# Kernel tuning notes

Measured on AMD Instinct MI355X. Metric: run time of the kernel, lower is better.

The kernel has to match this reference:

```python
import jax, jax.numpy as jnp
import numpy as np

N = 16384
D_IN = 1024
HID = [512, 512, 256]
N_PAIRS = 100000
N_CLS = 3


def setup_inputs() -> dict:
    key = jax.random.key(0)
    ks = jax.random.split(key, 16)
    x = jax.random.normal(ks[0], (N, D_IN), dtype=jnp.float32)
    adj = jax.random.uniform(ks[1], (N, N), dtype=jnp.float32) / N  # dense normalized adjacency
    tf_idx = jax.random.randint(ks[2], (N_PAIRS,), 0, N)
    gene_idx = jax.random.randint(ks[3], (N_PAIRS,), 0, N)
    # GCN layer weights
    W0 = jax.random.normal(ks[4], (D_IN, HID[0]), dtype=jnp.float32) / np.sqrt(D_IN)
    b0 = jnp.zeros((HID[0],), dtype=jnp.float32)
    W1 = jax.random.normal(ks[5], (HID[0], HID[1]), dtype=jnp.float32) / np.sqrt(HID[0])
    b1 = jnp.zeros((HID[1],), dtype=jnp.float32)
    W2 = jax.random.normal(ks[6], (HID[1], HID[2]), dtype=jnp.float32) / np.sqrt(HID[1])
    b2 = jnp.zeros((HID[2],), dtype=jnp.float32)
    # MLP head: Linear(2*256 -> 256), GELU, Linear(256 -> 3)
    Wh1 = jax.random.normal(ks[7], (2 * HID[2], HID[2]), dtype=jnp.float32) / np.sqrt(2 * HID[2])
    bh1 = jnp.zeros((HID[2],), dtype=jnp.float32)
    Wh2 = jax.random.normal(ks[8], (HID[2], N_CLS), dtype=jnp.float32) / np.sqrt(HID[2])
    bh2 = jnp.zeros((N_CLS,), dtype=jnp.float32)
    return {"x": x, "adj": adj, "tf_idx": tf_idx, "gene_idx": gene_idx,
            "W0": W0, "b0": b0, "W1": W1, "b1": b1, "W2": W2, "b2": b2,
            "Wh1": Wh1, "bh1": bh1, "Wh2": Wh2, "bh2": bh2}


def reference(x, adj, tf_idx, gene_idx, W0, b0, W1, b1, W2, b2, Wh1, bh1, Wh2, bh2):
    # GCNConv: out = adj @ (x @ W) + b; ReLU between layers (dropout off in eval)
    h = jax.nn.relu(adj @ (x @ W0) + b0)          # [N, 512]
    h = jax.nn.relu(adj @ (h @ W1) + b1)          # [N, 512]
    emb = adj @ (h @ W2) + b2                      # [N, 256]
    pair = jnp.concatenate([emb[tf_idx], emb[gene_idx]], axis=-1)  # [P, 512]
    hdn = jax.nn.gelu(pair @ Wh1 + bh1, approximate=False)          # [P, 256]
    logits = hdn @ Wh2 + bh2                                        # [P, 3]
    return logits
```

## Files before the change

### kernel.cpp

```cpp
#include <hip/hip_runtime.h>
#include <hip/hip_bf16.h>
#include <stdint.h>


using f32x4  = __attribute__((ext_vector_type(4))) float;
using bf16x8 = __attribute__((ext_vector_type(8))) __bf16;
using u16x8  = __attribute__((ext_vector_type(8))) unsigned short;
using u16x4  = __attribute__((ext_vector_type(4))) unsigned short;

static __device__ __forceinline__ unsigned short f2bf(float f) {
  unsigned u = __builtin_bit_cast(unsigned, f);
  u += 0x7FFFu + ((u >> 16) & 1u);
  return (unsigned short)(u >> 16);
}
static __device__ __forceinline__ float bf2f(unsigned short h) {
  unsigned u = ((unsigned)h) << 16;
  return __builtin_bit_cast(float, u);
}
static __device__ __forceinline__ void gload_lds16(const void* g, void* l) {
  __builtin_amdgcn_global_load_lds((__attribute__((address_space(1))) void*)(void*)g,
                                   (__attribute__((address_space(3))) void*)l,
                                   16, 0, 0);
}


__global__ void tcvt_kernel(const float* __restrict__ in,
                            unsigned short* __restrict__ outp, int K, int Nf) {
  int id = blockIdx.x * 256 + threadIdx.x;
  if (id >= K * Nf) return;
  int k = id % K, nf = id / K;
  outp[id] = f2bf(in[(size_t)k * Nf + nf]);
}

__global__ void cvt_bf16_kernel(const float* __restrict__ in,
                                unsigned short* __restrict__ outp, size_t n) {
  size_t i = ((size_t)blockIdx.x * blockDim.x + threadIdx.x) * 8;
  size_t stride = (size_t)gridDim.x * blockDim.x * 8;
  for (; i + 8 <= n; i += stride) {
    const float4* p = (const float4*)(in + i);
    float4 a = p[0], b = p[1];
    u16x8 v;
    v[0] = f2bf(a.x); v[1] = f2bf(a.y); v[2] = f2bf(a.z); v[3] = f2bf(a.w);
    v[4] = f2bf(b.x); v[5] = f2bf(b.y); v[6] = f2bf(b.z); v[7] = f2bf(b.w);
    *(u16x8*)(outp + i) = v;
  }
}

template <int NPART, bool RELU>
__global__ void reduceK_kernel(const float* __restrict__ Pp, const float* __restrict__ bias,
                               unsigned short* __restrict__ outp, int MN, int Nmask) {
  int i = (blockIdx.x * 256 + threadIdx.x) * 4;
  if (i >= MN) return;
  float4 s = *(const float4*)(Pp + i);
#pragma unroll
  for (int p = 1; p < NPART; ++p) {
    float4 v = *(const float4*)(Pp + (size_t)p * MN + i);
    s.x += v.x; s.y += v.y; s.z += v.z; s.w += v.w;
  }
  int col = i & Nmask;
  float r0 = s.x + bias[col + 0];
  float r1 = s.y + bias[col + 1];
  float r2 = s.z + bias[col + 2];
  float r3 = s.w + bias[col + 3];
  if (RELU) {
    r0 = fmaxf(r0, 0.0f); r1 = fmaxf(r1, 0.0f);
    r2 = fmaxf(r2, 0.0f); r3 = fmaxf(r3, 0.0f);
  }
  u16x4 o;
  o[0] = f2bf(r0); o[1] = f2bf(r1); o[2] = f2bf(r2); o[3] = f2bf(r3);
  *(u16x4*)(outp + i) = o;
}

__global__ __launch_bounds__(512, 1)
void gemm256(const unsigned short* __restrict__ A, const unsigned short* __restrict__ Bt,
             float* __restrict__ Pp, int M, int N, int K, int nbx, int Klen) {
  __shared__ __align__(16) unsigned short As[4 * 256 * 32];
  __shared__ __align__(16) unsigned short Bs[4 * 256 * 32];
  const int t = threadIdx.x, l = t & 63, w = t >> 6;

  int wg = blockIdx.x;
  const int cpx = gridDim.x >> 3;
  wg = (wg & 7) * cpx + (wg >> 3);
  const int mb = wg / nbx, nb = wg % nbx;
  const int kc = blockIdx.y;
  const int koff = kc * Klen;
  const int wr = w >> 2, wc = w & 3;
  const int fr = l & 15, fq = l >> 4;

  const int srow = t >> 2;
  const int sk0  = (t & 3) * 8;
  const unsigned short* AgR = A  + (size_t)(mb * 256 + srow) * K + koff + sk0;
  const unsigned short* BgR = Bt + (size_t)(nb * 256 + srow) * K + koff + sk0;
  unsigned short* AsL = As + t * 8;
  unsigned short* BsL = Bs + t * 8;

  const int NT = Klen >> 5;

#pragma unroll
  for (int s = 0; s < 3; ++s) {
    gload_lds16(AgR + s * 32, AsL + s * 8192);
    gload_lds16(AgR + (size_t)128 * K + s * 32, AsL + s * 8192 + 4096);
    gload_lds16(BgR + s * 32, BsL + s * 8192);
    gload_lds16(BgR + (size_t)128 * K + s * 32, BsL + s * 8192 + 4096);
  }
  asm volatile("s_waitcnt vmcnt(8)" ::: "memory");
  __builtin_amdgcn_sched_barrier(0);
  __builtin_amdgcn_s_barrier();

  f32x4 acc[8][4] = {};
  for (int tt = 0; tt < NT; ++tt) {
    const int buf = tt & 3;
    const int sb  = (tt + 3) & 3;
    const unsigned short* Ab = As + buf * 8192;
    const unsigned short* Bb = Bs + buf * 8192;
    const bool stg = (tt + 3) < NT;
    const unsigned short* AgS = AgR + (size_t)(tt + 3) * 32;
    const unsigned short* BgS = BgR + (size_t)(tt + 3) * 32;

    bf16x8 bfr[4], af[4];
#pragma unroll
    for (int ni = 0; ni < 4; ++ni)
      bfr[ni] = *(const bf16x8*)&Bb[(wc * 64 + ni * 16 + fr) * 32 + fq * 8];
#pragma unroll
    for (int mi = 0; mi < 4; ++mi)
      af[mi] = *(const bf16x8*)&Ab[(wr * 128 + mi * 16 + fr) * 32 + fq * 8];
    if (stg) {
      gload_lds16(AgS, AsL + sb * 8192);
      gload_lds16(AgS + (size_t)128 * K, AsL + sb * 8192 + 4096);
    }
    __builtin_amdgcn_sched_barrier(0);
    __builtin_amdgcn_s_barrier();
    asm volatile("s_waitcnt lgkmcnt(0)" ::: "memory");
    __builtin_amdgcn_sched_barrier(0);
    __builtin_amdgcn_s_setprio(1);
#pragma unroll
    for (int mi = 0; mi < 4; ++mi)
#pragma unroll
      for (int ni = 0; ni < 4; ++ni)
        acc[mi][ni] = __builtin_amdgcn_mfma_f32_16x16x32_bf16(af[mi], bfr[ni],
                                                              acc[mi][ni], 0, 0, 0);
    __builtin_amdgcn_s_setprio(0);
    __builtin_amdgcn_sched_barrier(0);
    __builtin_amdgcn_s_barrier();

    bf16x8 ag[4];
#pragma unroll
    for (int mi = 0; mi < 4; ++mi)
      ag[mi] = *(const bf16x8*)&Ab[(wr * 128 + (mi + 4) * 16 + fr) * 32 + fq * 8];
    if (stg) {
      gload_lds16(BgS, BsL + sb * 8192);
      gload_lds16(BgS + (size_t)128 * K, BsL + sb * 8192 + 4096);
    }
    __builtin_amdgcn_sched_barrier(0);
    __builtin_amdgcn_s_barrier();
    asm volatile("s_waitcnt lgkmcnt(0)" ::: "memory");
    __builtin_amdgcn_sched_barrier(0);
    __builtin_amdgcn_s_setprio(1);
#pragma unroll
    for (int mi = 0; mi < 4; ++mi)
#pragma unroll
      for (int ni = 0; ni < 4; ++ni)
        acc[mi + 4][ni] = __builtin_amdgcn_mfma_f32_16x16x32_bf16(ag[mi], bfr[ni],
                                                                  acc[mi + 4][ni], 0, 0, 0);
    __builtin_amdgcn_s_setprio(0);
    __builtin_amdgcn_sched_barrier(0);

    if (tt + 4 <= NT) {
      asm volatile("s_waitcnt vmcnt(8)" ::: "memory");
    } else if (tt + 3 == NT) {
      asm volatile("s_waitcnt vmcnt(4)" ::: "memory");
    } else {
      asm volatile("s_waitcnt vmcnt(0)" ::: "memory");
    }
    __builtin_amdgcn_sched_barrier(0);
    __builtin_amdgcn_s_barrier();
  }

  float* C = Pp + (size_t)kc * M * N;
  const int growb = mb * 256 + wr * 128 + fq * 4;
  const int gcolb = nb * 256 + wc * 64 + fr;
#pragma unroll
  for (int mi = 0; mi < 8; ++mi) {
    int row = growb + mi * 16;
#pragma unroll
    for (int ni = 0; ni < 4; ++ni) {
      int col = gcolb + ni * 16;
      f32x4 v = acc[mi][ni];
#pragma unroll
      for (int r = 0; r < 4; ++r)
        C[(size_t)(row + r) * N + col] = v[r];
    }
  }
}

template <int EP, bool ABF16>
__global__ __launch_bounds__(256, 2)
void gemm_bt(const void* __restrict__ Av, const unsigned short* __restrict__ Bt,
             void* __restrict__ Cout, const float* __restrict__ bias,
             int M, int N, int K, int nbx, int Klen) {
  __shared__ __align__(16) unsigned short As[128 * 64];
  __shared__ __align__(16) unsigned short Bs[128 * 64];
  const int t = threadIdx.x;
  const int l = t & 63;
  const int w = t >> 6;

  int wg = blockIdx.x;
  const int cpx = gridDim.x >> 3;
  wg = (wg & 7) * cpx + (wg >> 3);
  const int mb = wg / nbx, nb = wg % nbx;
  const int kc = blockIdx.y;
  const int koff = kc * Klen;

  const int wr = w >> 1, wc = w & 1;
  f32x4 acc[4][4] = {};

  const int srow = w * 8 + (l >> 3);
  const int sk0  = 8 * ((l & 7) ^ (l >> 3));
  const unsigned short* Bg = Bt + (size_t)(nb * 128 + srow) * K + koff + sk0;
  unsigned short* BsL = Bs + w * 512 + l * 8;
  unsigned short* AsL = As + w * 512 + l * 8;

  const unsigned short* Ag16 = nullptr;
  const float* Ag32 = nullptr;
  unsigned short* AsWr = nullptr;
  int ak = 0, axm = 0;
  if constexpr (ABF16) {
    Ag16 = (const unsigned short*)Av + (size_t)(mb * 128 + srow) * K + koff + sk0;
  } else {
    const int ar = t >> 1;
    ak = (t & 1) * 32;
    axm = (ar & 7) << 3;
    Ag32 = (const float*)Av + (size_t)(mb * 128 + ar) * K + koff + ak;
    AsWr = As + ar * 64;
  }

  const int fr = l & 15, fq = l >> 4;
  const int rxor = (fr & 7) << 3;

  const int steps = Klen >> 6;
  for (int kb = 0; kb < steps; ++kb) {
#pragma unroll
    for (int i = 0; i < 4; ++i)
      gload_lds16(Bg + (size_t)i * 32 * K, BsL + i * 2048);
    Bg += 64;
    if constexpr (ABF16) {
#pragma unroll
      for (int i = 0; i < 4; ++i)
        gload_lds16(Ag16 + (size_t)i * 32 * K, AsL + i * 2048);
      Ag16 += 64;
    } else {
#pragma unroll
      for (int q = 0; q < 4; ++q) {
        float4 c0 = ((const float4*)Ag32)[q * 2];
        float4 c1 = ((const float4*)Ag32)[q * 2 + 1];
        u16x8 v;
        v[0] = f2bf(c0.x); v[1] = f2bf(c0.y); v[2] = f2bf(c0.z); v[3] = f2bf(c0.w);
        v[4] = f2bf(c1.x); v[5] = f2bf(c1.y); v[6] = f2bf(c1.z); v[7] = f2bf(c1.w);
        *(u16x8*)&AsWr[(ak + q * 8) ^ axm] = v;
      }
      Ag32 += 64;
    }
    __syncthreads();

    bf16x8 af[2][4], bfr[2][4];
#pragma unroll
    for (int kk = 0; kk < 2; ++kk) {
#pragma unroll
      for (int mi = 0; mi < 4; ++mi) {
        int arow = wr * 64 + mi * 16 + fr;
        af[kk][mi] = *(const bf16x8*)&As[arow * 64 + ((kk * 32 + fq * 8) ^ rxor)];
      }
#pragma unroll
      for (int ni = 0; ni < 4; ++ni) {
        int brow = wc * 64 + ni * 16 + fr;
        bfr[kk][ni] = *(const bf16x8*)&Bs[brow * 64 + ((kk * 32 + fq * 8) ^ rxor)];
      }
    }
#pragma unroll
    for (int kk = 0; kk < 2; ++kk)
#pragma unroll
      for (int mi = 0; mi < 4; ++mi)
#pragma unroll
        for (int ni = 0; ni < 4; ++ni)
          acc[mi][ni] = __builtin_amdgcn_mfma_f32_16x16x32_bf16(af[kk][mi], bfr[kk][ni],
                                                                acc[mi][ni], 0, 0, 0);
    __syncthreads();
  }

  const int r0 = fq * 4;
  const int c0 = fr;
  const int growb = mb * 128 + wr * 64 + r0;
  const int gcolb = nb * 128 + wc * 64 + c0;
  if constexpr (EP == 0) {
    unsigned short* Ct = (unsigned short*)Cout;
#pragma unroll
    for (int ni = 0; ni < 4; ++ni) {
      int col = gcolb + ni * 16;
#pragma unroll
      for (int mi = 0; mi < 4; ++mi) {
        int row = growb + mi * 16;
        f32x4 v = acc[mi][ni];
        u16x4 o;
        o[0] = f2bf(v[0]); o[1] = f2bf(v[1]); o[2] = f2bf(v[2]); o[3] = f2bf(v[3]);
        *(u16x4*)&Ct[(size_t)col * M + row] = o;
      }
    }
  } else if constexpr (EP == 1) {
    unsigned short* C = (unsigned short*)Cout;
#pragma unroll
    for (int ni = 0; ni < 4; ++ni) {
      int col = gcolb + ni * 16;
      float b = bias[col];
#pragma unroll
      for (int mi = 0; mi < 4; ++mi) {
        int row = growb + mi * 16;
        f32x4 v = acc[mi][ni];
#pragma unroll
        for (int r = 0; r < 4; ++r)
          C[(size_t)(row + r) * N + col] = f2bf(fmaxf(v[r] + b, 0.0f));
      }
    }
  } else {
    float* C = (float*)Cout + (size_t)kc * M * N;
#pragma unroll
    for (int ni = 0; ni < 4; ++ni) {
      int col = gcolb + ni * 16;
#pragma unroll
      for (int mi = 0; mi < 4; ++mi) {
        int row = growb + mi * 16;
        f32x4 v = acc[mi][ni];
#pragma unroll
        for (int r = 0; r < 4; ++r)
          C[(size_t)(row + r) * N + col] = v[r];
      }
    }
  }
}

__global__ __launch_bounds__(256, 2)
void head_kernel(const unsigned short* __restrict__ EMB, const int* __restrict__ tf,
                 const int* __restrict__ gi, const unsigned short* __restrict__ Wh1t,
                 const float* __restrict__ bh1, const float* __restrict__ Wh2,
                 const float* __restrict__ bh2, float* __restrict__ out, int P) {
  __shared__ __align__(16) union SU {
    struct { unsigned short As[64 * 64]; unsigned short Bs[256 * 64]; } s;
    unsigned short hdn[64 * 264];
  } u;
  __shared__ float wh2s[256 * 3];
  const int t = threadIdx.x, l = t & 63, w = t >> 6;
  const int pb = blockIdx.x;

  wh2s[t]       = Wh2[t];
  wh2s[t + 256] = Wh2[t + 256];
  wh2s[t + 512] = Wh2[t + 512];

  const int srow = w * 8 + (l >> 3);
  const int sk0  = 8 * ((l & 7) ^ (l >> 3));
  size_t tfo[2], gio[2];
#pragma unroll
  for (int i = 0; i < 2; ++i) {
    int p = pb * 64 + i * 32 + srow;
    if (p >= P) p = P - 1;
    tfo[i] = (size_t)tf[p] * 256;
    gio[i] = (size_t)gi[p] * 256;
  }
  const unsigned short* BgB = Wh1t + (size_t)srow * 512 + sk0;
  unsigned short* AsL = u.s.As + w * 512 + l * 8;
  unsigned short* BsL = u.s.Bs + w * 512 + l * 8;

  const int fr = l & 15, fq = l >> 4;
  const int rxor = (fr & 7) << 3;

  f32x4 acc[4][4] = {};
  for (int kb = 0; kb < 8; ++kb) {
    const int klo = (kb & 3) * 64 + sk0;
#pragma unroll
    for (int i = 0; i < 2; ++i)
      gload_lds16(EMB + ((kb < 4) ? tfo[i] : gio[i]) + klo, AsL + i * 2048);
#pragma unroll
    for (int i = 0; i < 8; ++i)
      gload_lds16(BgB + (size_t)i * 32 * 512 + kb * 64, BsL + i * 2048);
    __syncthreads();

    bf16x8 af[2][4], bfr[2][4];
#pragma unroll
    for (int kk = 0; kk < 2; ++kk) {
#pragma unroll
      for (int mi = 0; mi < 4; ++mi) {
        int arow = mi * 16 + fr;
        af[kk][mi] = *(const bf16x8*)&u.s.As[arow * 64 + ((kk * 32 + fq * 8) ^ rxor)];
      }
#pragma unroll
      for (int ni = 0; ni < 4; ++ni) {
        int brow = w * 64 + ni * 16 + fr;
        bfr[kk][ni] = *(const bf16x8*)&u.s.Bs[brow * 64 + ((kk * 32 + fq * 8) ^ rxor)];
      }
    }
#pragma unroll
    for (int kk = 0; kk < 2; ++kk)
#pragma unroll
      for (int mi = 0; mi < 4; ++mi)
#pragma unroll
        for (int ni = 0; ni < 4; ++ni)
          acc[mi][ni] = __builtin_amdgcn_mfma_f32_16x16x32_bf16(af[kk][mi], bfr[kk][ni],
                                                                acc[mi][ni], 0, 0, 0);
    __syncthreads();
  }

  const int r0 = fq * 4, c0 = fr;
#pragma unroll
  for (int ni = 0; ni < 4; ++ni) {
    int col = w * 64 + ni * 16 + c0;
    float b = bh1[col];
#pragma unroll
    for (int mi = 0; mi < 4; ++mi) {
      int row = mi * 16 + r0;
      f32x4 v = acc[mi][ni];
#pragma unroll
      for (int r = 0; r < 4; ++r) {
        float xv = v[r] + b;
        float g = 0.5f * xv * (1.0f + erff(xv * 0.70710678118f));
        u.hdn[(row + r) * 264 + col] = f2bf(g);
      }
    }
  }
  __syncthreads();

  const int pl = w * 16 + (l >> 2);
  const int pg = pb * 64 + pl;
  const int ks = (l & 3) * 64;
  float a0 = 0.f, a1 = 0.f, a2 = 0.f;
  const unsigned short* hr = u.hdn + pl * 264 + ks;
#pragma unroll
  for (int kq = 0; kq < 8; ++kq) {
    u16x8 hv = *(const u16x8*)(hr + kq * 8);
#pragma unroll
    for (int j = 0; j < 8; ++j) {
      float h = bf2f(hv[j]);
      int k = ks + kq * 8 + j;
      a0 = fmaf(h, wh2s[k * 3 + 0], a0);
      a1 = fmaf(h, wh2s[k * 3 + 1], a1);
      a2 = fmaf(h, wh2s[k * 3 + 2], a2);
    }
  }
  a0 += __shfl_xor(a0, 1); a0 += __shfl_xor(a0, 2);
  a1 += __shfl_xor(a1, 1); a1 += __shfl_xor(a1, 2);
  a2 += __shfl_xor(a2, 1); a2 += __shfl_xor(a2, 2);
  if ((l & 3) == 0 && pg < P) {
    out[(size_t)pg * 3 + 0] = a0 + bh2[0];
    out[(size_t)pg * 3 + 1] = a1 + bh2[1];
    out[(size_t)pg * 3 + 2] = a2 + bh2[2];
  }
}


extern "C" void kernel_launch(void* const* d_in, const int* in_sizes, int n_in,
                              void* d_out, int out_size, void* d_ws, size_t ws_size,
                              hipStream_t stream) {
  const float* x   = (const float*)d_in[0];
  const float* adj = (const float*)d_in[1];
  const int*   tf  = (const int*)d_in[2];
  const int*   gi  = (const int*)d_in[3];
  const float* W0  = (const float*)d_in[4];
  const float* b0  = (const float*)d_in[5];
  const float* W1  = (const float*)d_in[6];
  const float* b1  = (const float*)d_in[7];
  const float* W2  = (const float*)d_in[8];
  const float* b2  = (const float*)d_in[9];
  const float* Wh1 = (const float*)d_in[10];
  const float* bh1 = (const float*)d_in[11];
  const float* Wh2 = (const float*)d_in[12];
  const float* bh2 = (const float*)d_in[13];
  float* out = (float*)d_out;

  const int NN = 16384;
  const int P = in_sizes[2];

  char* ws = (char*)d_ws;
  size_t off = 0;
  auto alloc = [&](size_t bytes) -> char* {
    char* p = ws + off;
    off += (bytes + 255) & ~(size_t)255;
    return p;
  };
  unsigned short* W0t  = (unsigned short*)alloc((size_t)512 * 1024 * 2);
  unsigned short* W1t  = (unsigned short*)alloc((size_t)512 * 512 * 2);
  unsigned short* W2t  = (unsigned short*)alloc((size_t)256 * 512 * 2);
  unsigned short* Wh1t = (unsigned short*)alloc((size_t)256 * 512 * 2);
  unsigned short* Tt   = (unsigned short*)alloc((size_t)512 * NN * 2);
  unsigned short* H    = (unsigned short*)alloc((size_t)NN * 512 * 2);
  unsigned short* EMB  = (unsigned short*)alloc((size_t)NN * 256 * 2);
  float*          Pp   = (float*)alloc((size_t)2 * NN * 512 * 4);
  size_t base_end = off;

  bool useAdjB = false;
  unsigned short* adjb = nullptr;
  if (ws_size >= base_end + (size_t)NN * NN * 2) {
    adjb = (unsigned short*)alloc((size_t)NN * NN * 2);
    useAdjB = true;
  }

  tcvt_kernel<<<dim3((1024 * 512 + 255) / 256), 256, 0, stream>>>(W0, W0t, 1024, 512);
  tcvt_kernel<<<dim3((512 * 512 + 255) / 256), 256, 0, stream>>>(W1, W1t, 512, 512);
  tcvt_kernel<<<dim3((512 * 256 + 255) / 256), 256, 0, stream>>>(W2, W2t, 512, 256);
  tcvt_kernel<<<dim3((512 * 256 + 255) / 256), 256, 0, stream>>>(Wh1, Wh1t, 512, 256);
  if (useAdjB)
    cvt_bf16_kernel<<<4096, 256, 0, stream>>>(adj, adjb, (size_t)NN * NN);

  gemm_bt<0, false><<<dim3(512), 256, 0, stream>>>(x, W0t, Tt, nullptr,
                                                   NN, 512, 1024, 4, 1024);
  if (useAdjB) {
    gemm256<<<dim3(128, 2), 512, 0, stream>>>(adjb, Tt, Pp, NN, 512, NN, 2, NN / 2);
    reduceK_kernel<2, true><<<dim3(8192), 256, 0, stream>>>(Pp, b0, H, NN * 512, 511);
  } else {
    gemm_bt<1, false><<<dim3(512), 256, 0, stream>>>(adj, Tt, H, b0,
                                                     NN, 512, NN, 4, NN);
  }
  gemm_bt<0, true><<<dim3(512), 256, 0, stream>>>(H, W1t, Tt, nullptr,
                                                  NN, 512, 512, 4, 512);
  if (useAdjB) {
    gemm256<<<dim3(128, 2), 512, 0, stream>>>(adjb, Tt, Pp, NN, 512, NN, 2, NN / 2);
    reduceK_kernel<2, true><<<dim3(8192), 256, 0, stream>>>(Pp, b1, H, NN * 512, 511);
  } else {
    gemm_bt<1, false><<<dim3(512), 256, 0, stream>>>(adj, Tt, H, b1,
                                                     NN, 512, NN, 4, NN);
  }
  gemm_bt<0, true><<<dim3(256), 256, 0, stream>>>(H, W2t, Tt, nullptr,
                                                  NN, 256, 512, 2, 512);
  if (useAdjB) {
    gemm256<<<dim3(64, 4), 512, 0, stream>>>(adjb, Tt, Pp, NN, 256, NN, 1, NN / 4);
    reduceK_kernel<4, false><<<dim3(4096), 256, 0, stream>>>(Pp, b2, EMB, NN * 256, 255);
  } else {
    gemm_bt<3, false><<<dim3(256, 2), 256, 0, stream>>>(adj, Tt, Pp, nullptr,
                                                        NN, 256, NN, 2, NN / 2);
    reduceK_kernel<2, false><<<dim3(4096), 256, 0, stream>>>(Pp, b2, EMB, NN * 256, 255);
  }
  head_kernel<<<dim3((P + 63) / 64), 256, 0, stream>>>(EMB, tf, gi, Wh1t, bh1,
                                                       Wh2, bh2, out, P);
}
```

Measured before the change: 1.289 ms.

## Software-pipeline LDS fragment reads and cut GEMM loop to one barrier per K-step

New measurement: 1.311 ms. About the same (+1.7%).

```diff
diff --git a/kernel.cpp b/kernel.cpp
--- a/kernel.cpp
+++ b/kernel.cpp
@@ -96,85 +96,87 @@
 
   const int NT = Klen >> 5;
 
-#pragma unroll
-  for (int s = 0; s < 3; ++s) {
-    gload_lds16(AgR + s * 32, AsL + s * 8192);
-    gload_lds16(AgR + (size_t)128 * K + s * 32, AsL + s * 8192 + 4096);
-    gload_lds16(BgR + s * 32, BsL + s * 8192);
-    gload_lds16(BgR + (size_t)128 * K + s * 32, BsL + s * 8192 + 4096);
-  }
-  asm volatile("s_waitcnt vmcnt(8)" ::: "memory");
+  const int aoff = (wr * 128 + fr) * 32 + fq * 8;
+  const int boff = (wc * 64 + fr) * 32 + fq * 8;
+
+#define STAGE_A(s)                                                            \
+  { gload_lds16(AgR + (size_t)(s) * 32, AsL + ((s) & 3) * 8192);              \
+    gload_lds16(AgR + (size_t)128 * K + (size_t)(s) * 32,                     \
+                AsL + ((s) & 3) * 8192 + 4096); }
+#define STAGE_B(s)                                                            \
+  { gload_lds16(BgR + (size_t)(s) * 32, BsL + ((s) & 3) * 8192);              \
+    gload_lds16(BgR + (size_t)128 * K + (size_t)(s) * 32,                     \
+                BsL + ((s) & 3) * 8192 + 4096); }
+#define READ_B(dst, u)                                                        \
+  _Pragma("unroll")                                                           \
+  for (int ni = 0; ni < 4; ++ni)                                              \
+    dst[ni] = *(const bf16x8*)&Bs[((u) & 3) * 8192 + boff + ni * 512];
+#define READ_A03(dst, u)                                                      \
+  _Pragma("unroll")                                                           \
+  for (int mi = 0; mi < 4; ++mi)                                              \
+    dst[mi] = *(const bf16x8*)&As[((u) & 3) * 8192 + aoff + mi * 512];
+#define READ_A47(dst, u)                                                      \
+  _Pragma("unroll")                                                           \
+  for (int mi = 0; mi < 4; ++mi)                                              \
+    dst[mi] = *(const bf16x8*)&As[((u) & 3) * 8192 + aoff + 2048 + mi * 512];
+
+#pragma unroll
+  for (int s = 0; s < 3; ++s) { STAGE_A(s); STAGE_B(s); }
+  asm volatile("s_waitcnt vmcnt(4)" ::: "memory");
   __builtin_amdgcn_sched_barrier(0);
   __builtin_amdgcn_s_barrier();
 
+  bf16x8 bA[4], aA[4], bB[4], aB[4], a47[4];
+  READ_B(bA, 0);
+  READ_A03(aA, 0);
+
   f32x4 acc[8][4] = {};
-  for (int tt = 0; tt < NT; ++tt) {
-    const int buf = tt & 3;
-    const int sb  = (tt + 3) & 3;
-    const unsigned short* Ab = As + buf * 8192;
-    const unsigned short* Bb = Bs + buf * 8192;
-    const bool stg = (tt + 3) < NT;
-    const unsigned short* AgS = AgR + (size_t)(tt + 3) * 32;
-    const unsigned short* BgS = BgR + (size_t)(tt + 3) * 32;
-
-    bf16x8 bfr[4], af[4];
-#pragma unroll
-    for (int ni = 0; ni < 4; ++ni)
-      bfr[ni] = *(const bf16x8*)&Bb[(wc * 64 + ni * 16 + fr) * 32 + fq * 8];
-#pragma unroll
-    for (int mi = 0; mi < 4; ++mi)
-      af[mi] = *(const bf16x8*)&Ab[(wr * 128 + mi * 16 + fr) * 32 + fq * 8];
-    if (stg) {
-      gload_lds16(AgS, AsL + sb * 8192);
-      gload_lds16(AgS + (size_t)128 * K, AsL + sb * 8192 + 4096);
-    }
-    __builtin_amdgcn_sched_barrier(0);
-    __builtin_amdgcn_s_barrier();
-    asm volatile("s_waitcnt lgkmcnt(0)" ::: "memory");
-    __builtin_amdgcn_sched_barrier(0);
-    __builtin_amdgcn_s_setprio(1);
-#pragma unroll
-    for (int mi = 0; mi < 4; ++mi)
-#pragma unroll
-      for (int ni = 0; ni < 4; ++ni)
-        acc[mi][ni] = __builtin_amdgcn_mfma_f32_16x16x32_bf16(af[mi], bfr[ni],
-                                                              acc[mi][ni], 0, 0, 0);
-    __builtin_amdgcn_s_setprio(0);
-    __builtin_amdgcn_sched_barrier(0);
-    __builtin_amdgcn_s_barrier();
-
-    bf16x8 ag[4];
-#pragma unroll
-    for (int mi = 0; mi < 4; ++mi)
-      ag[mi] = *(const bf16x8*)&Ab[(wr * 128 + (mi + 4) * 16 + fr) * 32 + fq * 8];
-    if (stg) {
-      gload_lds16(BgS, BsL + sb * 8192);
-      gload_lds16(BgS + (size_t)128 * K, BsL + sb * 8192 + 4096);
-    }
-    __builtin_amdgcn_sched_barrier(0);
-    __builtin_amdgcn_s_barrier();
-    asm volatile("s_waitcnt lgkmcnt(0)" ::: "memory");
-    __builtin_amdgcn_sched_barrier(0);
-    __builtin_amdgcn_s_setprio(1);
-#pragma unroll
-    for (int mi = 0; mi < 4; ++mi)
-#pragma unroll
-      for (int ni = 0; ni < 4; ++ni)
-        acc[mi + 4][ni] = __builtin_amdgcn_mfma_f32_16x16x32_bf16(ag[mi], bfr[ni],
-                                                                  acc[mi + 4][ni], 0, 0, 0);
-    __builtin_amdgcn_s_setprio(0);
-    __builtin_amdgcn_sched_barrier(0);
-
-    if (tt + 4 <= NT) {
-      asm volatile("s_waitcnt vmcnt(8)" ::: "memory");
-    } else if (tt + 3 == NT) {
-      asm volatile("s_waitcnt vmcnt(4)" ::: "memory");
-    } else {
-      asm volatile("s_waitcnt vmcnt(0)" ::: "memory");
-    }
-    __builtin_amdgcn_sched_barrier(0);
-    __builtin_amdgcn_s_barrier();
-  }
+
+#define SUBTILE(CB, CA, NB, NA, u)                                            \
+  {                                                                           \
+    asm volatile("s_waitcnt lgkmcnt(0)" ::: "memory");                        \
+    __builtin_amdgcn_sched_barrier(0);                                        \
+    READ_A47(a47, (u));                                                       \
+    __builtin_amdgcn_s_setprio(1);                                            \
+    _Pragma("unroll")                                                         \
+    for (int mi = 0; mi < 4; ++mi)                                            \
+      _Pragma("unroll")                                                       \
+      for (int ni = 0; ni < 4; ++ni)                                          \
+        acc[mi][ni] = __builtin_amdgcn_mfma_f32_16x16x32_bf16(                \
+            CA[mi], CB[ni], acc[mi][ni], 0, 0, 0);                            \
+    __builtin_amdgcn_s_setprio(0);                                            \
+    if ((u) + 3 < NT) STAGE_A((u) + 3);                                       \
+    asm volatile("s_waitcnt lgkmcnt(0)" ::: "memory");                        \
+    __builtin_amdgcn_sched_barrier(0);                                        \
+    __builtin_amdgcn_s_setprio(1);                                            \
+    _Pragma("unroll")                                                         \
+    for (int mi = 0; mi < 4; ++mi)                                            \
+      _Pragma("unroll")                                                       \
+      for (int ni = 0; ni < 4; ++ni)                                          \
+        acc[mi + 4][ni] = __builtin_amdgcn_mfma_f32_16x16x32_bf16(            \
+            a47[mi], CB[ni], acc[mi + 4][ni], 0, 0, 0);                       \
+    __builtin_amdgcn_s_setprio(0);                                            \
+    if ((u) + 1 < NT) { READ_B(NB, (u) + 1); READ_A03(NA, (u) + 1); }         \
+    if ((u) + 3 < NT) STAGE_B((u) + 3);                                       \
+    if ((u) + 3 < NT) {                                                       \
+      asm volatile("s_waitcnt vmcnt(4)" ::: "memory");                        \
+    } else {                                                                  \
+      asm volatile("s_waitcnt vmcnt(0)" ::: "memory");                        \
+    }                                                                         \
+    __builtin_amdgcn_sched_barrier(0);                                        \
+    __builtin_amdgcn_s_barrier();                                             \
+  }
+
+  for (int tt = 0; tt < NT; tt += 2) {
+    SUBTILE(bA, aA, bB, aB, tt);
+    SUBTILE(bB, aB, bA, aA, tt + 1);
+  }
+#undef SUBTILE
+#undef READ_A47
+#undef READ_A03
+#undef READ_B
+#undef STAGE_B
+#undef STAGE_A
 
   float* C = Pp + (size_t)kc * M * N;
   const int growb = mb * 256 + wr * 128 + fq * 4;
```

## Replace 256x256 adjacency GEMM with full-N-width 128-row tiles and 3-stage pipeline

Applied to the files above, without the earlier changes.

Measured after the change: 1.324 ms. 1.03x slower.

```diff
diff --git a/kernel.cpp b/kernel.cpp
--- a/kernel.cpp
+++ b/kernel.cpp
@@ -71,119 +71,101 @@
   *(u16x4*)(outp + i) = o;
 }
 
-__global__ __launch_bounds__(512, 1)
-void gemm256(const unsigned short* __restrict__ A, const unsigned short* __restrict__ Bt,
-             float* __restrict__ Pp, int M, int N, int K, int nbx, int Klen) {
-  __shared__ __align__(16) unsigned short As[4 * 256 * 32];
-  __shared__ __align__(16) unsigned short Bs[4 * 256 * 32];
+template <int NI>
+__global__ __launch_bounds__(512, 2)
+void gemmA(const unsigned short* __restrict__ A, const unsigned short* __restrict__ Bt,
+           float* __restrict__ Pp, int M, int N, int K) {
+  constexpr int NL = 1 + NI;
+  __shared__ __align__(16) unsigned short As[3 * 128 * 32];
+  __shared__ __align__(16) unsigned short Bs[3 * NI * 128 * 32];
   const int t = threadIdx.x, l = t & 63, w = t >> 6;
 
-  int wg = blockIdx.x;
-  const int cpx = gridDim.x >> 3;
-  wg = (wg & 7) * cpx + (wg >> 3);
-  const int mb = wg / nbx, nb = wg % nbx;
-  const int kc = blockIdx.y;
+  const int wg = (blockIdx.x & 7) * 32 + (blockIdx.x >> 3);
+  const int kc = wg >> 7;
+  const int mb = wg & 127;
+  const int Klen = K >> 1;
   const int koff = kc * Klen;
-  const int wr = w >> 2, wc = w & 3;
+  const int NT = Klen >> 5;
   const int fr = l & 15, fq = l >> 4;
 
-  const int srow = t >> 2;
-  const int sk0  = (t & 3) * 8;
-  const unsigned short* AgR = A  + (size_t)(mb * 256 + srow) * K + koff + sk0;
-  const unsigned short* BgR = Bt + (size_t)(nb * 256 + srow) * K + koff + sk0;
+  const unsigned short* AgR = A  + (size_t)(mb * 128 + (t >> 2)) * K + koff + (t & 3) * 8;
+  const unsigned short* BgR = Bt + (size_t)(t >> 2) * K + koff + (t & 3) * 8;
   unsigned short* AsL = As + t * 8;
   unsigned short* BsL = Bs + t * 8;
 
-  const int NT = Klen >> 5;
-
-#pragma unroll
-  for (int s = 0; s < 3; ++s) {
-    gload_lds16(AgR + s * 32, AsL + s * 8192);
-    gload_lds16(AgR + (size_t)128 * K + s * 32, AsL + s * 8192 + 4096);
-    gload_lds16(BgR + s * 32, BsL + s * 8192);
-    gload_lds16(BgR + (size_t)128 * K + s * 32, BsL + s * 8192 + 4096);
-  }
-  asm volatile("s_waitcnt vmcnt(8)" ::: "memory");
+#define STAGE_A(s, b)  gload_lds16(AgR + (size_t)(s) * 32, AsL + (b) * 4096);
+#define STAGE_B(s, b)                                                         \
+  _Pragma("unroll")                                                           \
+  for (int j = 0; j < NI; ++j)                                                \
+    gload_lds16(BgR + (size_t)(j * 128) * K + (size_t)(s) * 32,               \
+                BsL + (b) * NI * 4096 + j * 4096);
+
+  STAGE_A(0, 0) STAGE_B(0, 0)
+  STAGE_A(1, 1) STAGE_B(1, 1)
+  asm volatile("s_waitcnt vmcnt(%0)" :: "i"(NL) : "memory");
   __builtin_amdgcn_sched_barrier(0);
   __builtin_amdgcn_s_barrier();
 
-  f32x4 acc[8][4] = {};
+  f32x4 acc[8][NI] = {};
+  const int aoff = fr * 32 + fq * 8;
+  const int boff = (w * (NI * 16) + fr) * 32 + fq * 8;
+
+  int bb = 0, sb = 2;
   for (int tt = 0; tt < NT; ++tt) {
-    const int buf = tt & 3;
-    const int sb  = (tt + 3) & 3;
-    const unsigned short* Ab = As + buf * 8192;
-    const unsigned short* Bb = Bs + buf * 8192;
-    const bool stg = (tt + 3) < NT;
-    const unsigned short* AgS = AgR + (size_t)(tt + 3) * 32;
-    const unsigned short* BgS = BgR + (size_t)(tt + 3) * 32;
-
-    bf16x8 bfr[4], af[4];
-#pragma unroll
-    for (int ni = 0; ni < 4; ++ni)
-      bfr[ni] = *(const bf16x8*)&Bb[(wc * 64 + ni * 16 + fr) * 32 + fq * 8];
+    const bool stg = (tt + 2) < NT;
+    bf16x8 a03[4], a47[4], bf[NI];
 #pragma unroll
     for (int mi = 0; mi < 4; ++mi)
-      af[mi] = *(const bf16x8*)&Ab[(wr * 128 + mi * 16 + fr) * 32 + fq * 8];
-    if (stg) {
-      gload_lds16(AgS, AsL + sb * 8192);
-      gload_lds16(AgS + (size_t)128 * K, AsL + sb * 8192 + 4096);
-    }
+      a03[mi] = *(const bf16x8*)&As[bb * 4096 + aoff + mi * 512];
+#pragma unroll
+    for (int ni = 0; ni < NI; ++ni)
+      bf[ni] = *(const bf16x8*)&Bs[bb * NI * 4096 + boff + ni * 512];
+#pragma unroll
+    for (int mi = 0; mi < 4; ++mi)
+      a47[mi] = *(const bf16x8*)&As[bb * 4096 + aoff + 2048 + mi * 512];
+    if (stg) { STAGE_A(tt + 2, sb) }
+    asm volatile("s_waitcnt lgkmcnt(4)" ::: "memory");
     __builtin_amdgcn_sched_barrier(0);
-    __builtin_amdgcn_s_barrier();
+    __builtin_amdgcn_s_setprio(1);
+#pragma unroll
+    for (int mi = 0; mi < 4; ++mi)
+#pragma unroll
+      for (int ni = 0; ni < NI; ++ni)
+        acc[mi][ni] = __builtin_amdgcn_mfma_f32_16x16x32_bf16(a03[mi], bf[ni],
+                                                              acc[mi][ni], 0, 0, 0);
+    __builtin_amdgcn_s_setprio(0);
     asm volatile("s_waitcnt lgkmcnt(0)" ::: "memory");
     __builtin_amdgcn_sched_barrier(0);
     __builtin_amdgcn_s_setprio(1);
 #pragma unroll
     for (int mi = 0; mi < 4; ++mi)
 #pragma unroll
-      for (int ni = 0; ni < 4; ++ni)
-        acc[mi][ni] = __builtin_amdgcn_mfma_f32_16x16x32_bf16(af[mi], bfr[ni],
-                                                              acc[mi][ni], 0, 0, 0);
+      for (int ni = 0; ni < NI; ++ni)
+        acc[mi + 4][ni] = __builtin_amdgcn_mfma_f32_16x16x32_bf16(a47[mi], bf[ni],
+                                                                  acc[mi + 4][ni], 0, 0, 0);
     __builtin_amdgcn_s_setprio(0);
+    if (stg) { STAGE_B(tt + 2, sb) }
+    if (stg) {
+      asm volatile("s_waitcnt vmcnt(%0)" :: "i"(NL) : "memory");
+    } else {
+      asm volatile("s_waitcnt vmcnt(0)" ::: "memory");
+    }
     __builtin_amdgcn_sched_barrier(0);
     __builtin_amdgcn_s_barrier();
-
-    bf16x8 ag[4];
-#pragma unroll
-    for (int mi = 0; mi < 4; ++mi)
-      ag[mi] = *(const bf16x8*)&Ab[(wr * 128 + (mi + 4) * 16 + fr) * 32 + fq * 8];
-    if (stg) {
-      gload_lds16(BgS, BsL + sb * 8192);
-      gload_lds16(BgS + (size_t)128 * K, BsL + sb * 8192 + 4096);
-    }
-    __builtin_amdgcn_sched_barrier(0);
-    __builtin_amdgcn_s_barrier();
-    asm volatile("s_waitcnt lgkmcnt(0)" ::: "memory");
-    __builtin_amdgcn_sched_barrier(0);
-    __builtin_amdgcn_s_setprio(1);
-#pragma unroll
-    for (int mi = 0; mi < 4; ++mi)
-#pragma unroll
-      for (int ni = 0; ni < 4; ++ni)
-        acc[mi + 4][ni] = __builtin_amdgcn_mfma_f32_16x16x32_bf16(ag[mi], bfr[ni],
-                                                                  acc[mi + 4][ni], 0, 0, 0);
-    __builtin_amdgcn_s_setprio(0);
-    __builtin_amdgcn_sched_barrier(0);
-
-    if (tt + 4 <= NT) {
-      asm volatile("s_waitcnt vmcnt(8)" ::: "memory");
-    } else if (tt + 3 == NT) {
-      asm volatile("s_waitcnt vmcnt(4)" ::: "memory");
-    } else {
-      asm volatile("s_waitcnt vmcnt(0)" ::: "memory");
-    }
-    __builtin_amdgcn_sched_barrier(0);
-    __builtin_amdgcn_s_barrier();
-  }
+    bb = (bb == 2) ? 0 : bb + 1;
+    sb = (sb == 2) ? 0 : sb + 1;
+  }
+#undef STAGE_B
+#undef STAGE_A
 
   float* C = Pp + (size_t)kc * M * N;
-  const int growb = mb * 256 + wr * 128 + fq * 4;
-  const int gcolb = nb * 256 + wc * 64 + fr;
+  const int growb = mb * 128 + fq * 4;
+  const int gcolb = w * (NI * 16) + fr;
 #pragma unroll
   for (int mi = 0; mi < 8; ++mi) {
     int row = growb + mi * 16;
 #pragma unroll
-    for (int ni = 0; ni < 4; ++ni) {
+    for (int ni = 0; ni < NI; ++ni) {
       int col = gcolb + ni * 16;
       f32x4 v = acc[mi][ni];
 #pragma unroll
@@ -510,7 +492,7 @@
   gemm_bt<0, false><<<dim3(512), 256, 0, stream>>>(x, W0t, Tt, nullptr,
                                                    NN, 512, 1024, 4, 1024);
   if (useAdjB) {
-    gemm256<<<dim3(128, 2), 512, 0, stream>>>(adjb, Tt, Pp, NN, 512, NN, 2, NN / 2);
+    gemmA<4><<<dim3(256), 512, 0, stream>>>(adjb, Tt, Pp, NN, 512, NN);
     reduceK_kernel<2, true><<<dim3(8192), 256, 0, stream>>>(Pp, b0, H, NN * 512, 511);
   } else {
     gemm_bt<1, false><<<dim3(512), 256, 0, stream>>>(adj, Tt, H, b0,
@@ -519,7 +501,7 @@
   gemm_bt<0, true><<<dim3(512), 256, 0, stream>>>(H, W1t, Tt, nullptr,
                                                   NN, 512, 512, 4, 512);
   if (useAdjB) {
-    gemm256<<<dim3(128, 2), 512, 0, stream>>>(adjb, Tt, Pp, NN, 512, NN, 2, NN / 2);
+    gemmA<4><<<dim3(256), 512, 0, stream>>>(adjb, Tt, Pp, NN, 512, NN);
     reduceK_kernel<2, true><<<dim3(8192), 256, 0, stream>>>(Pp, b1, H, NN * 512, 511);
   } else {
     gemm_bt<1, false><<<dim3(512), 256, 0, stream>>>(adj, Tt, H, b1,
@@ -528,8 +510,8 @@
   gemm_bt<0, true><<<dim3(256), 256, 0, stream>>>(H, W2t, Tt, nullptr,
                                                   NN, 256, 512, 2, 512);
   if (useAdjB) {
-    gemm256<<<dim3(64, 4), 512, 0, stream>>>(adjb, Tt, Pp, NN, 256, NN, 1, NN / 4);
-    reduceK_kernel<4, false><<<dim3(4096), 256, 0, stream>>>(Pp, b2, EMB, NN * 256, 255);
+    gemmA<2><<<dim3(256), 512, 0, stream>>>(adjb, Tt, Pp, NN, 256, NN);
+    reduceK_kernel<2, false><<<dim3(4096), 256, 0, stream>>>(Pp, b2, EMB, NN * 256, 255);
   } else {
     gemm_bt<3, false><<<dim3(256, 2), 256, 0, stream>>>(adj, Tt, Pp, nullptr,
                                                         NN, 256, NN, 2, NN / 2);
```
